# Kernel tuning notes

Hardware: AMD Instinct MI355X
Metric: run time of the kernel (lower is better)

Reference implementation:

```python
import jax, jax.numpy as jnp
import numpy as np

N_WIRES = 4


def _apply_rx(state, theta, wire):
    """Apply RX(theta) on `wire`. state: [B] + [2]*n complex; theta: [B] or scalar.
    RX(t) = cos(t/2) I - i sin(t/2) X, and X flips the wire axis."""
    n = state.ndim - 1
    half = theta * 0.5
    c = jnp.cos(half).astype(jnp.complex64)
    s = jnp.sin(half).astype(jnp.complex64)
    c = jnp.reshape(c, jnp.shape(c) + (1,) * n)
    s = jnp.reshape(s, jnp.shape(s) + (1,) * n)
    return c * state - 1j * s * jnp.flip(state, axis=wire + 1)


def _apply_cnot(state, control, target):
    """CNOT: flip target axis on the control=1 slice."""
    s0 = jax.lax.index_in_dim(state, 0, axis=control + 1, keepdims=True)
    s1 = jax.lax.index_in_dim(state, 1, axis=control + 1, keepdims=True)
    s1 = jnp.flip(s1, axis=target + 1)
    return jnp.concatenate([s0, s1], axis=control + 1)


def _encode(data, theta):
    """data: [B, n_wires] float angles -> [B, 2**n_wires] complex state."""
    B = data.shape[0]
    state = jnp.zeros((B,) + (2,) * N_WIRES, dtype=jnp.complex64)
    state = state.at[(slice(None),) + (0,) * N_WIRES].set(1.0)  # |0...0>
    for w in range(N_WIRES):              # data encoding RX per wire
        state = _apply_rx(state, data[:, w], w)
    for w in range(N_WIRES):              # trainable RX per wire
        state = _apply_rx(state, theta[w], w)
    for w in range(N_WIRES - 1):          # CNOT ladder
        state = _apply_cnot(state, w, w + 1)
    return state.reshape(B, 2 ** N_WIRES)


def setup_inputs() -> dict:
    key = jax.random.key(0)
    kx, ky, kt = jax.random.split(key, 3)
    x = jax.random.normal(kx, (8192, 4), dtype=jnp.float32)
    y = jax.random.normal(ky, (8192, 4), dtype=jnp.float32)
    theta = jax.random.normal(kt, (4,), dtype=jnp.float32)
    return {"x": x, "y": y, "theta": theta}


def reference(x, y, theta):
    states_x = _encode(x, theta)  # [Bx, 16] complex64
    states_y = _encode(y, theta)  # [By, 16] complex64
    # Faithful to torch source: plain matmul (no conjugate), then abs.
    return jnp.abs(states_x @ states_y.T)  # [Bx, By] float32
```

## Files before the change

### kernel.cpp

```cpp
#include <hip/hip_runtime.h>
#include <math.h>


#define BM 16
#define BN 256

__global__ __launch_bounds__(256) void qk_main(
    const float* __restrict__ x, const float* __restrict__ y,
    const float* __restrict__ theta, float* __restrict__ out,
    int Bx, int By)
{
    __shared__ float at[8][BM];
    __shared__ float bt[8][BN];

    const int tid = threadIdx.x;
    const int i0 = blockIdx.y * BM;
    const int j0 = blockIdx.x * BN;

    const float th0 = 0.5f * theta[0];
    const float th1 = 0.5f * theta[1];
    const float th2 = 0.5f * theta[2];
    const float th3 = 0.5f * theta[3];

    {
        const float4 y4 = ((const float4*)y)[j0 + tid];
        float s, c;
        __sincosf(0.5f * y4.x + th0, &s, &c); bt[0][tid] = c; bt[4][tid] = s;
        __sincosf(0.5f * y4.y + th1, &s, &c); bt[1][tid] = c; bt[5][tid] = s;
        __sincosf(0.5f * y4.z + th2, &s, &c); bt[2][tid] = c; bt[6][tid] = s;
        __sincosf(0.5f * y4.w + th3, &s, &c); bt[3][tid] = c; bt[7][tid] = s;
    }
    if (tid < BM) {
        const float4 x4 = ((const float4*)x)[i0 + tid];
        float s, c;
        __sincosf(0.5f * x4.x + th0, &s, &c); at[0][tid] = c; at[4][tid] = s;
        __sincosf(0.5f * x4.y + th1, &s, &c); at[1][tid] = c; at[5][tid] = s;
        __sincosf(0.5f * x4.z + th2, &s, &c); at[2][tid] = c; at[6][tid] = s;
        __sincosf(0.5f * x4.w + th3, &s, &c); at[3][tid] = c; at[7][tid] = s;
    }
    __syncthreads();

    const int tx = tid & 63;
    const int ty = tid >> 6;

    float acc[4][4];
    #pragma unroll
    for (int w = 0; w < 4; ++w) {
        const float4 ca = ((const float4*)&at[w][0])[ty];
        const float4 sa = ((const float4*)&at[w + 4][0])[ty];
        const float4 cb = ((const float4*)&bt[w][0])[tx];
        const float4 sb = ((const float4*)&bt[w + 4][0])[tx];

        const float cai[4] = {ca.x, ca.y, ca.z, ca.w};
        const float sai[4] = {sa.x, sa.y, sa.z, sa.w};
        const float cbj[4] = {cb.x, cb.y, cb.z, cb.w};
        const float sbj[4] = {sb.x, sb.y, sb.z, sb.w};

        #pragma unroll
        for (int i = 0; i < 4; ++i) {
            #pragma unroll
            for (int j = 0; j < 4; ++j) {
                const float t = fmaf(cai[i], cbj[j], -(sai[i] * sbj[j]));
                acc[i][j] = (w == 0) ? t : acc[i][j] * t;
            }
        }
    }

    #pragma unroll
    for (int i = 0; i < 4; ++i) {
        const int row = i0 + ty * 4 + i;
        float4 o;
        o.x = fabsf(acc[i][0]);
        o.y = fabsf(acc[i][1]);
        o.z = fabsf(acc[i][2]);
        o.w = fabsf(acc[i][3]);
        ((float4*)&out[(size_t)row * By + j0])[tx] = o;
    }
}

extern "C" void kernel_launch(void* const* d_in, const int* in_sizes, int n_in,
                              void* d_out, int out_size, void* d_ws, size_t ws_size,
                              hipStream_t stream) {
    const float* x     = (const float*)d_in[0];
    const float* y     = (const float*)d_in[1];
    const float* theta = (const float*)d_in[2];
    float* out = (float*)d_out;

    const int Bx = in_sizes[0] / 4;
    const int By = in_sizes[1] / 4;

    dim3 grid(By / BN, Bx / BM);
    qk_main<<<grid, dim3(256), 0, stream>>>(x, y, theta, out, Bx, By);
}
```

Baseline: 251.1 us.

## Precompute trig tables in a prologue kernel and loop chunks per block

Moves the per-element sincos of x and y into a separate pre-pass kernel that writes cos/sin tables to workspace. The main kernel then reads those tables from global memory, with no shared memory or barrier. Each block keeps its 16 x-rows in registers and walks eight 256-column chunks of y, so far fewer blocks are launched. The aim is to remove redundant sincos work and per-block setup in a store-bound kernel. In exchange it adds a second launch and workspace traffic, and it hardcodes N=8192.

```diff
diff --git a/kernel.cpp b/kernel.cpp
--- a/kernel.cpp
+++ b/kernel.cpp
@@ -2,79 +2,99 @@
 #include <math.h>
 
 
-#define BM 16
-#define BN 256
+#define N 8192
+#define ROWS_PER_STRIPE 16
+#define CHUNK 256
+#define WALKERS 4
+#define CHUNKS_PER_WALKER 8
 
-__global__ __launch_bounds__(256) void qk_main(
+
+__global__ __launch_bounds__(256) void qk_trig(
     const float* __restrict__ x, const float* __restrict__ y,
-    const float* __restrict__ theta, float* __restrict__ out,
-    int Bx, int By)
+    const float* __restrict__ theta, float* __restrict__ ws)
 {
-    __shared__ float at[8][BM];
-    __shared__ float bt[8][BN];
-
-    const int tid = threadIdx.x;
-    const int i0 = blockIdx.y * BM;
-    const int j0 = blockIdx.x * BN;
-
+    const int r = blockIdx.x * 256 + threadIdx.x;
     const float th0 = 0.5f * theta[0];
     const float th1 = 0.5f * theta[1];
     const float th2 = 0.5f * theta[2];
     const float th3 = 0.5f * theta[3];
 
-    {
-        const float4 y4 = ((const float4*)y)[j0 + tid];
-        float s, c;
-        __sincosf(0.5f * y4.x + th0, &s, &c); bt[0][tid] = c; bt[4][tid] = s;
-        __sincosf(0.5f * y4.y + th1, &s, &c); bt[1][tid] = c; bt[5][tid] = s;
-        __sincosf(0.5f * y4.z + th2, &s, &c); bt[2][tid] = c; bt[6][tid] = s;
-        __sincosf(0.5f * y4.w + th3, &s, &c); bt[3][tid] = c; bt[7][tid] = s;
-    }
-    if (tid < BM) {
-        const float4 x4 = ((const float4*)x)[i0 + tid];
-        float s, c;
-        __sincosf(0.5f * x4.x + th0, &s, &c); at[0][tid] = c; at[4][tid] = s;
-        __sincosf(0.5f * x4.y + th1, &s, &c); at[1][tid] = c; at[5][tid] = s;
-        __sincosf(0.5f * x4.z + th2, &s, &c); at[2][tid] = c; at[6][tid] = s;
-        __sincosf(0.5f * x4.w + th3, &s, &c); at[3][tid] = c; at[7][tid] = s;
-    }
-    __syncthreads();
+    const bool is_y = (r >= N);
+    const int row = is_y ? (r - N) : r;
+    const float4 v = ((const float4*)(is_y ? y : x))[row];
+    float* base = ws + (is_y ? 8 * N : 0);
 
+    float s, c;
+    __sincosf(0.5f * v.x + th0, &s, &c); base[0 * N + row] = c; base[4 * N + row] = s;
+    __sincosf(0.5f * v.y + th1, &s, &c); base[1 * N + row] = c; base[5 * N + row] = s;
+    __sincosf(0.5f * v.z + th2, &s, &c); base[2 * N + row] = c; base[6 * N + row] = s;
+    __sincosf(0.5f * v.w + th3, &s, &c); base[3 * N + row] = c; base[7 * N + row] = s;
+}
+
+__global__ __launch_bounds__(256) void qk_main(
+    const float* __restrict__ ws, float* __restrict__ out)
+{
+    const int tid = threadIdx.x;
     const int tx = tid & 63;
     const int ty = tid >> 6;
+    const int stripe = blockIdx.x >> 2;
+    const int cw = blockIdx.x & (WALKERS - 1);
 
-    float acc[4][4];
+    const int row0 = stripe * ROWS_PER_STRIPE + ty * 4;
+
+    const float* xc = ws;
+    const float* xs = ws + 4 * N;
+    const float* yc = ws + 8 * N;
+    const float* ys = ws + 12 * N;
+
+    float4 ac[4], as4[4];
     #pragma unroll
     for (int w = 0; w < 4; ++w) {
-        const float4 ca = ((const float4*)&at[w][0])[ty];
-        const float4 sa = ((const float4*)&at[w + 4][0])[ty];
-        const float4 cb = ((const float4*)&bt[w][0])[tx];
-        const float4 sb = ((const float4*)&bt[w + 4][0])[tx];
+        ac[w]  = *(const float4*)&xc[w * N + row0];
+        as4[w] = *(const float4*)&xs[w * N + row0];
+    }
+    const float cai[4][4] = {
+        {ac[0].x, ac[0].y, ac[0].z, ac[0].w}, {ac[1].x, ac[1].y, ac[1].z, ac[1].w},
+        {ac[2].x, ac[2].y, ac[2].z, ac[2].w}, {ac[3].x, ac[3].y, ac[3].z, ac[3].w}};
+    const float sai[4][4] = {
+        {as4[0].x, as4[0].y, as4[0].z, as4[0].w}, {as4[1].x, as4[1].y, as4[1].z, as4[1].w},
+        {as4[2].x, as4[2].y, as4[2].z, as4[2].w}, {as4[3].x, as4[3].y, as4[3].z, as4[3].w}};
 
-        const float cai[4] = {ca.x, ca.y, ca.z, ca.w};
-        const float sai[4] = {sa.x, sa.y, sa.z, sa.w};
-        const float cbj[4] = {cb.x, cb.y, cb.z, cb.w};
-        const float sbj[4] = {sb.x, sb.y, sb.z, sb.w};
+    #pragma unroll 1
+    for (int k = 0; k < CHUNKS_PER_WALKER; ++k) {
+        const int j0 = (cw * CHUNKS_PER_WALKER + k) * CHUNK + tx * 4;
+
+        float4 bc[4], bs4[4];
+        #pragma unroll
+        for (int w = 0; w < 4; ++w) {
+            bc[w]  = *(const float4*)&yc[w * N + j0];
+            bs4[w] = *(const float4*)&ys[w * N + j0];
+        }
+
+        float acc[4][4];
+        #pragma unroll
+        for (int w = 0; w < 4; ++w) {
+            const float cbj[4] = {bc[w].x, bc[w].y, bc[w].z, bc[w].w};
+            const float sbj[4] = {bs4[w].x, bs4[w].y, bs4[w].z, bs4[w].w};
+            #pragma unroll
+            for (int i = 0; i < 4; ++i) {
+                #pragma unroll
+                for (int j = 0; j < 4; ++j) {
+                    const float t = fmaf(cai[w][i], cbj[j], -(sai[w][i] * sbj[j]));
+                    acc[i][j] = (w == 0) ? t : acc[i][j] * t;
+                }
+            }
+        }
 
         #pragma unroll
         for (int i = 0; i < 4; ++i) {
-            #pragma unroll
-            for (int j = 0; j < 4; ++j) {
-                const float t = fmaf(cai[i], cbj[j], -(sai[i] * sbj[j]));
-                acc[i][j] = (w == 0) ? t : acc[i][j] * t;
-            }
+            float4 o;
+            o.x = fabsf(acc[i][0]);
+            o.y = fabsf(acc[i][1]);
+            o.z = fabsf(acc[i][2]);
+            o.w = fabsf(acc[i][3]);
+            *(float4*)&out[(size_t)(row0 + i) * N + j0] = o;
         }
-    }
-
-    #pragma unroll
-    for (int i = 0; i < 4; ++i) {
-        const int row = i0 + ty * 4 + i;
-        float4 o;
-        o.x = fabsf(acc[i][0]);
-        o.y = fabsf(acc[i][1]);
-        o.z = fabsf(acc[i][2]);
-        o.w = fabsf(acc[i][3]);
-        ((float4*)&out[(size_t)row * By + j0])[tx] = o;
     }
 }
 
@@ -85,10 +105,9 @@
     const float* y     = (const float*)d_in[1];
     const float* theta = (const float*)d_in[2];
     float* out = (float*)d_out;
+    float* ws  = (float*)d_ws;
 
-    const int Bx = in_sizes[0] / 4;
-    const int By = in_sizes[1] / 4;
+    qk_trig<<<(2 * N) / 256, 256, 0, stream>>>(x, y, theta, ws);
 
-    dim3 grid(By / BN, Bx / BM);
-    qk_main<<<grid, dim3(256), 0, stream>>>(x, y, theta, out, Bx, By);
+    qk_main<<<(N / ROWS_PER_STRIPE) * WALKERS, 256, 0, stream>>>(ws, out);
 }
```

Measured after the change: 308.8 us. 1.23x slower.
